# Performance work log

Hardware: AMD Instinct MI355X
Metric: run time of the kernel (lower is better)

The kernel has to match this reference:

```python
import jax, jax.numpy as jnp
import numpy as np

B, C, H, W = 4, 256, 64, 64
C8 = C // 8


def setup_inputs() -> dict:
    key = jax.random.key(0)
    ks = jax.random.split(key, 8)
    x = jax.random.normal(ks[0], (B, C, H, W), dtype=jnp.float32)
    # 1x1 conv weights act as per-pixel linear maps: [out_ch, in_ch]
    Wq = jax.random.normal(ks[1], (C8, C), dtype=jnp.float32) * 0.05
    bq = jax.random.normal(ks[2], (C8,), dtype=jnp.float32) * 0.01
    Wk = jax.random.normal(ks[3], (C8, C), dtype=jnp.float32) * 0.05
    bk = jax.random.normal(ks[4], (C8,), dtype=jnp.float32) * 0.01
    Wv = jax.random.normal(ks[5], (C, C), dtype=jnp.float32) * 0.05
    bv = jax.random.normal(ks[6], (C,), dtype=jnp.float32) * 0.01
    # torch inits gamma to 0 (identity); use nonzero so output exercises the attention path
    gamma = jnp.array(0.5, dtype=jnp.float32)
    return {"x": x, "Wq": Wq, "bq": bq, "Wk": Wk, "bk": bk, "Wv": Wv, "bv": bv, "gamma": gamma}


def reference(x, Wq, bq, Wk, bk, Wv, bv, gamma):
    b, c, h, w = x.shape
    n = h * w
    xf = x.reshape(b, c, n)                                   # [B,C,N]
    q = jnp.einsum('oc,bcn->bno', Wq, xf) + bq                # [B,N,C8] (proj_query permuted)
    k = jnp.einsum('oc,bcn->bon', Wk, xf) + bk[:, None]       # [B,C8,N]
    energy = jnp.einsum('bnc,bcm->bnm', q, k)                 # [B,N_q,N_k]
    # NOTE: torch Softmax(dim=1) -> normalize over the QUERY axis (axis=1)
    attention = jax.nn.softmax(energy, axis=1)
    v = jnp.einsum('oc,bcn->bon', Wv, xf) + bv[:, None]       # [B,C,N]
    out = jnp.einsum('bcn,bnm->bcm', v, attention).reshape(b, c, h, w)
    return gamma * out + x
```

## Files before the change

kernel.cpp:

```cpp
#include <hip/hip_runtime.h>
#include <hip/hip_bf16.h>

#define BN 4
#define CC 256
#define C8 32
#define NN 4096
#define PROJ_ROWS 320

typedef __attribute__((ext_vector_type(8))) short short8;
typedef __attribute__((ext_vector_type(4))) float f32x4;

__device__ __forceinline__ unsigned short f2bf(float f) {
    unsigned u = __builtin_bit_cast(unsigned, f);
    unsigned r = (u + 0x7fffu + ((u >> 16) & 1u)) >> 16;
    return (unsigned short)r;
}

__global__ __launch_bounds__(256) void proj_kernel(
    const float* __restrict__ x,
    const float* __restrict__ Wq, const float* __restrict__ bq,
    const float* __restrict__ Wk, const float* __restrict__ bk,
    const float* __restrict__ Wv, const float* __restrict__ bv,
    unsigned short* __restrict__ proj, unsigned short* __restrict__ qT)
{
    int bid = blockIdx.x;
    int b = bid >> 6, nt = bid & 63;
    int n0 = nt * 64;
    int tid = threadIdx.x;
    int w = tid >> 6, l = tid & 63, l15 = l & 15, lq = l >> 4;

    __shared__ alignas(16) unsigned short Xt[64][264];

    int c_l = tid >> 3;
    int nb  = (tid & 7) * 8;

#pragma unroll
    for (int kc = 0; kc < 8; kc++) {
        const float* xp = x + ((size_t)(b * CC + kc * 32 + c_l)) * NN + n0 + nb;
        float4 x0 = *(const float4*)xp;
        float4 x1 = *(const float4*)(xp + 4);
        float t[8] = {x0.x, x0.y, x0.z, x0.w, x1.x, x1.y, x1.z, x1.w};
#pragma unroll
        for (int e = 0; e < 8; e++) Xt[nb + e][kc * 32 + c_l] = f2bf(t[e]);
    }
    __syncthreads();

    f32x4 acc[5][4];
#pragma unroll
    for (int gi = 0; gi < 5; gi++)
#pragma unroll
        for (int mi = 0; mi < 4; mi++) acc[gi][mi] = (f32x4){0.f, 0.f, 0.f, 0.f};

    for (int kc = 0; kc < 8; kc++) {
        float4 wf[5][2];
#pragma unroll
        for (int gi = 0; gi < 5; gi++) {
            int og = (w * 5 + gi) * 16 + l15;
            const float* wrow = (og < 32) ? (Wq + (size_t)og * CC)
                              : (og < 64) ? (Wk + (size_t)(og - 32) * CC)
                                          : (Wv + (size_t)(og - 64) * CC);
            const float* wp = wrow + kc * 32 + lq * 8;
            wf[gi][0] = *(const float4*)wp;
            wf[gi][1] = *(const float4*)(wp + 4);
        }
#pragma unroll
        for (int gi = 0; gi < 5; gi++) {
            unsigned short a8[8] __attribute__((aligned(16)));
            float tw[8] = {wf[gi][0].x, wf[gi][0].y, wf[gi][0].z, wf[gi][0].w,
                           wf[gi][1].x, wf[gi][1].y, wf[gi][1].z, wf[gi][1].w};
#pragma unroll
            for (int e = 0; e < 8; e++) a8[e] = f2bf(tw[e]);
            short8 af = *(const short8*)a8;
#pragma unroll
            for (int mi = 0; mi < 4; mi++) {
                short8 bf = *(const short8*)&Xt[mi * 16 + l15][kc * 32 + lq * 8];
                acc[gi][mi] = __builtin_amdgcn_mfma_f32_16x16x32_bf16(af, bf, acc[gi][mi], 0, 0, 0);
            }
        }
    }

#pragma unroll
    for (int gi = 0; gi < 5; gi++) {
#pragma unroll
        for (int r = 0; r < 4; r++) {
            int og = (w * 5 + gi) * 16 + lq * 4 + r;
            float bias = (og < 32) ? bq[og] : (og < 64) ? bk[og - 32] : bv[og - 64];
#pragma unroll
            for (int mi = 0; mi < 4; mi++) {
                int n = n0 + mi * 16 + l15;
                unsigned short v16 = f2bf(acc[gi][mi][r] + bias);
                if (og < 32) {
                    qT[((size_t)b * NN + n) * C8 + og] = v16;
                } else {
                    proj[((size_t)b * PROJ_ROWS + og) * NN + n] = v16;
                }
            }
        }
    }
}

template<int NSPLIT, bool FINAL>
__global__ __launch_bounds__(256, 4) void attn_kernel(
    const unsigned short* __restrict__ proj,
    const unsigned short* __restrict__ qT,
    const float* __restrict__ x,
    const float* __restrict__ gamma_p,
    float* __restrict__ out,
    float* __restrict__ Opart,
    float* __restrict__ Lpart)
{
    constexpr int ITERS = 64 / NSPLIT;
    int bid = blockIdx.x;
    int h   = bid >> 8;
    int low = bid & 255;
    int xcd = low & 7;
    int b = xcd >> 1;
    int mtile = ((low >> 3) << 1) | (xcd & 1);
    int m0 = mtile * 64;
    int nbase = h * (ITERS * 64);

    int tid = threadIdx.x;
    int w = tid >> 6, l = tid & 63, l15 = l & 15, lq = l >> 4;

    __shared__ alignas(16) unsigned short ps[2][64][72];
    __shared__ float red[4][64];
    __shared__ float Ltot[64];

    const unsigned short* kbase = proj + ((size_t)b * PROJ_ROWS + C8) * NN;
    const unsigned short* vbase = proj + ((size_t)b * PROJ_ROWS + 64) * NN;
    const unsigned short* qbase = qT + (size_t)b * NN * C8;

    short8 kfrag[4];
#pragma unroll
    for (int mi = 0; mi < 4; mi++) {
        int col = m0 + mi * 16 + l15;
        unsigned short t8[8] __attribute__((aligned(16)));
#pragma unroll
        for (int j = 0; j < 8; j++)
            t8[j] = kbase[(size_t)(lq * 8 + j) * NN + col];
        kfrag[mi] = *(const short8*)t8;
    }

    f32x4 O[4][4];
#pragma unroll
    for (int ci = 0; ci < 4; ci++)
#pragma unroll
        for (int mi = 0; mi < 4; mi++) O[ci][mi] = (f32x4){0.f, 0.f, 0.f, 0.f};
    float runS[4] = {0.f, 0.f, 0.f, 0.f};

    {
        short8 qfrag = *(const short8*)(qbase + (size_t)(nbase + 16 * w + l15) * C8 + lq * 8);
#pragma unroll
        for (int mi = 0; mi < 4; mi++) {
            f32x4 S = __builtin_amdgcn_mfma_f32_16x16x32_bf16(
                qfrag, kfrag[mi], (f32x4){0.f, 0.f, 0.f, 0.f}, 0, 0, 0);
            float p0 = __expf(S[0]);
            float p1 = __expf(S[1]);
            float p2 = __expf(S[2]);
            float p3 = __expf(S[3]);
            runS[mi] += (p0 + p1) + (p2 + p3);
            unsigned pk0 = (unsigned)f2bf(p0) | ((unsigned)f2bf(p1) << 16);
            unsigned pk1 = (unsigned)f2bf(p2) | ((unsigned)f2bf(p3) << 16);
            *(uint2*)&ps[0][mi * 16 + l15][16 * w + lq * 4] = make_uint2(pk0, pk1);
        }
    }

    for (int it = 0; it < ITERS; it++) {
        int n0c = nbase + it * 64;
        __syncthreads();

        const unsigned short* psrc = &ps[it & 1][0][0];
#pragma unroll
        for (int kh = 0; kh < 2; kh++) {
            short8 av[4];
#pragma unroll
            for (int ci = 0; ci < 4; ci++)
                av[ci] = *(const short8*)(vbase
                         + (size_t)(64 * w + ci * 16 + l15) * NN + n0c + kh * 32 + lq * 8);
            short8 bfr[4];
#pragma unroll
            for (int mi = 0; mi < 4; mi++)
                bfr[mi] = *(const short8*)(psrc + (mi * 16 + l15) * 72 + kh * 32 + lq * 8);
#pragma unroll
            for (int ci = 0; ci < 4; ci++)
#pragma unroll
                for (int mi = 0; mi < 4; mi++)
                    O[ci][mi] = __builtin_amdgcn_mfma_f32_16x16x32_bf16(
                        av[ci], bfr[mi], O[ci][mi], 0, 0, 0);
        }

        if (it + 1 < ITERS) {
            short8 qfrag = *(const short8*)(qbase
                           + (size_t)(n0c + 64 + 16 * w + l15) * C8 + lq * 8);
            unsigned short* pdst = &ps[(it + 1) & 1][0][0];
#pragma unroll
            for (int mi = 0; mi < 4; mi++) {
                f32x4 S = __builtin_amdgcn_mfma_f32_16x16x32_bf16(
                    qfrag, kfrag[mi], (f32x4){0.f, 0.f, 0.f, 0.f}, 0, 0, 0);
                float p0 = __expf(S[0]);
                float p1 = __expf(S[1]);
                float p2 = __expf(S[2]);
                float p3 = __expf(S[3]);
                runS[mi] += (p0 + p1) + (p2 + p3);
                unsigned pk0 = (unsigned)f2bf(p0) | ((unsigned)f2bf(p1) << 16);
                unsigned pk1 = (unsigned)f2bf(p2) | ((unsigned)f2bf(p3) << 16);
                *(uint2*)(pdst + (mi * 16 + l15) * 72 + 16 * w + lq * 4) = make_uint2(pk0, pk1);
            }
        }
    }

#pragma unroll
    for (int mi = 0; mi < 4; mi++) {
        float s = runS[mi];
        s += __shfl_xor(s, 16);
        s += __shfl_xor(s, 32);
        red[w][mi * 16 + l15] = s;
    }
    __syncthreads();
    if (tid < 64) Ltot[tid] = red[0][tid] + red[1][tid] + red[2][tid] + red[3][tid];
    __syncthreads();

    if constexpr (FINAL) {
        float gamma = gamma_p[0];
        float iv[4];
#pragma unroll
        for (int mi = 0; mi < 4; mi++) iv[mi] = 1.0f / Ltot[mi * 16 + l15];
#pragma unroll
        for (int ci = 0; ci < 4; ci++) {
#pragma unroll
            for (int mi = 0; mi < 4; mi++) {
                int m = m0 + mi * 16 + l15;
#pragma unroll
                for (int r = 0; r < 4; r++) {
                    int c = 64 * w + ci * 16 + lq * 4 + r;
                    size_t idx = ((size_t)b * CC + c) * NN + m;
                    out[idx] = gamma * (O[ci][mi][r] * iv[mi]) + x[idx];
                }
            }
        }
    } else {
        size_t p = ((size_t)h * BN + b) * 64 + mtile;
        if (tid < 64) Lpart[p * 64 + tid] = Ltot[tid];
        float* Ob = Opart + p * (size_t)(CC * 64);
#pragma unroll
        for (int ci = 0; ci < 4; ci++) {
#pragma unroll
            for (int mi = 0; mi < 4; mi++) {
#pragma unroll
                for (int r = 0; r < 4; r++) {
                    int c = 64 * w + ci * 16 + lq * 4 + r;
                    Ob[c * 64 + mi * 16 + l15] = O[ci][mi][r];
                }
            }
        }
    }
}

template<int NSPLIT>
__global__ __launch_bounds__(256) void combine_kernel(
    const float* __restrict__ Opart, const float* __restrict__ Lpart,
    const float* __restrict__ x, const float* __restrict__ gamma_p,
    float* __restrict__ out)
{
    int bid = blockIdx.x;
    int cq = bid & 3;
    int mt = (bid >> 2) & 63;
    int b  = bid >> 8;
    int tid = threadIdx.x;
    int m4 = tid & 15, c16 = tid >> 4;
    float gamma = gamma_p[0];

    f32x4 Ls = (f32x4){0.f, 0.f, 0.f, 0.f};
#pragma unroll
    for (int h = 0; h < NSPLIT; h++) {
        size_t p = ((size_t)h * BN + b) * 64 + mt;
        Ls += *(const f32x4*)(Lpart + p * 64 + m4 * 4);
    }
    f32x4 inv;
#pragma unroll
    for (int j = 0; j < 4; j++) inv[j] = 1.0f / Ls[j];

#pragma unroll
    for (int cp = 0; cp < 4; cp++) {
        int c = cq * 64 + cp * 16 + c16;
        f32x4 acc = (f32x4){0.f, 0.f, 0.f, 0.f};
#pragma unroll
        for (int h = 0; h < NSPLIT; h++) {
            size_t p = ((size_t)h * BN + b) * 64 + mt;
            acc += *(const f32x4*)(Opart + p * (size_t)(CC * 64) + c * 64 + m4 * 4);
        }
        size_t idx = ((size_t)b * CC + c) * NN + mt * 64 + m4 * 4;
        f32x4 xv = *(const f32x4*)(x + idx);
        f32x4 o;
#pragma unroll
        for (int j = 0; j < 4; j++) o[j] = gamma * (acc[j] * inv[j]) + xv[j];
        *(f32x4*)(out + idx) = o;
    }
}

extern "C" void kernel_launch(void* const* d_in, const int* in_sizes, int n_in,
                              void* d_out, int out_size, void* d_ws, size_t ws_size,
                              hipStream_t stream) {
    const float* x     = (const float*)d_in[0];
    const float* Wq    = (const float*)d_in[1];
    const float* bq    = (const float*)d_in[2];
    const float* Wk    = (const float*)d_in[3];
    const float* bk    = (const float*)d_in[4];
    const float* Wv    = (const float*)d_in[5];
    const float* bv    = (const float*)d_in[6];
    const float* gamma = (const float*)d_in[7];
    float* out = (float*)d_out;
    (void)in_sizes; (void)n_in; (void)out_size;

    unsigned short* proj = (unsigned short*)d_ws;
    unsigned short* qT   = proj + (size_t)BN * PROJ_ROWS * NN;
    const size_t baseB = ((size_t)BN * PROJ_ROWS * NN + (size_t)BN * NN * C8) * 2;

    auto needB = [&](int ns) {
        size_t LpB = (size_t)ns * BN * 64 * 64 * 4;
        size_t OpB = (size_t)ns * BN * 64 * CC * 64 * 4;
        return baseB + LpB + OpB;
    };

    proj_kernel<<<256, 256, 0, stream>>>(x, Wq, bq, Wk, bk, Wv, bv, proj, qT);

    if (ws_size >= needB(4)) {
        float* Lpart = (float*)((char*)d_ws + baseB);
        float* Opart = Lpart + (size_t)4 * BN * 64 * 64;
        attn_kernel<4, false><<<1024, 256, 0, stream>>>(proj, qT, x, gamma, out, Opart, Lpart);
        combine_kernel<4><<<1024, 256, 0, stream>>>(Opart, Lpart, x, gamma, out);
    } else if (ws_size >= needB(2)) {
        float* Lpart = (float*)((char*)d_ws + baseB);
        float* Opart = Lpart + (size_t)2 * BN * 64 * 64;
        attn_kernel<2, false><<<512, 256, 0, stream>>>(proj, qT, x, gamma, out, Opart, Lpart);
        combine_kernel<2><<<1024, 256, 0, stream>>>(Opart, Lpart, x, gamma, out);
    } else {
        attn_kernel<1, true><<<256, 256, 0, stream>>>(proj, qT, x, gamma, out, nullptr, nullptr);
    }
}
```

Before: 181.7 us.

## Split attention 8-way, store partials in bf16, fold log2e into K, halve proj tiles

The attention split-K factor goes from 4 to 8 (2048 blocks), with launch bounds raised to 8 waves per SIMD, and partial outputs are stored as bf16 to cut combine traffic. K is pre-scaled by log2(e) in the projection so the softmax can use exp2f. The projection kernel uses 32-column tiles and 512 blocks for more parallelism. Risks: bf16 partial sums lose precision, the higher occupancy target may cause register spills, and the NSPLIT=2 fallback is removed.

```diff
diff --git a/kernel.cpp b/kernel.cpp
--- a/kernel.cpp
+++ b/kernel.cpp
@@ -6,6 +6,7 @@
 #define C8 32
 #define NN 4096
 #define PROJ_ROWS 320
+#define LOG2E 1.4426950408889634f
 
 typedef __attribute__((ext_vector_type(8))) short short8;
 typedef __attribute__((ext_vector_type(4))) float f32x4;
@@ -14,6 +15,12 @@
     unsigned u = __builtin_bit_cast(unsigned, f);
     unsigned r = (u + 0x7fffu + ((u >> 16) & 1u)) >> 16;
     return (unsigned short)r;
+}
+__device__ __forceinline__ float bfhi2f(unsigned u) {
+    return __builtin_bit_cast(float, u & 0xffff0000u);
+}
+__device__ __forceinline__ float bflo2f(unsigned u) {
+    return __builtin_bit_cast(float, u << 16);
 }
 
 __global__ __launch_bounds__(256) void proj_kernel(
@@ -24,32 +31,32 @@
     unsigned short* __restrict__ proj, unsigned short* __restrict__ qT)
 {
     int bid = blockIdx.x;
-    int b = bid >> 6, nt = bid & 63;
-    int n0 = nt * 64;
+    int b = bid >> 7, nt = bid & 127;
+    int n0 = nt * 32;
     int tid = threadIdx.x;
     int w = tid >> 6, l = tid & 63, l15 = l & 15, lq = l >> 4;
 
-    __shared__ alignas(16) unsigned short Xt[64][264];
+    __shared__ alignas(16) unsigned short Xt[32][264];
 
     int c_l = tid >> 3;
-    int nb  = (tid & 7) * 8;
+    int nb  = (tid & 7) * 4;
 
 #pragma unroll
     for (int kc = 0; kc < 8; kc++) {
         const float* xp = x + ((size_t)(b * CC + kc * 32 + c_l)) * NN + n0 + nb;
         float4 x0 = *(const float4*)xp;
-        float4 x1 = *(const float4*)(xp + 4);
-        float t[8] = {x0.x, x0.y, x0.z, x0.w, x1.x, x1.y, x1.z, x1.w};
-#pragma unroll
-        for (int e = 0; e < 8; e++) Xt[nb + e][kc * 32 + c_l] = f2bf(t[e]);
+        Xt[nb + 0][kc * 32 + c_l] = f2bf(x0.x);
+        Xt[nb + 1][kc * 32 + c_l] = f2bf(x0.y);
+        Xt[nb + 2][kc * 32 + c_l] = f2bf(x0.z);
+        Xt[nb + 3][kc * 32 + c_l] = f2bf(x0.w);
     }
     __syncthreads();
 
-    f32x4 acc[5][4];
+    f32x4 acc[5][2];
 #pragma unroll
     for (int gi = 0; gi < 5; gi++)
 #pragma unroll
-        for (int mi = 0; mi < 4; mi++) acc[gi][mi] = (f32x4){0.f, 0.f, 0.f, 0.f};
+        for (int mi = 0; mi < 2; mi++) acc[gi][mi] = (f32x4){0.f, 0.f, 0.f, 0.f};
 
     for (int kc = 0; kc < 8; kc++) {
         float4 wf[5][2];
@@ -72,7 +79,7 @@
             for (int e = 0; e < 8; e++) a8[e] = f2bf(tw[e]);
             short8 af = *(const short8*)a8;
 #pragma unroll
-            for (int mi = 0; mi < 4; mi++) {
+            for (int mi = 0; mi < 2; mi++) {
                 short8 bf = *(const short8*)&Xt[mi * 16 + l15][kc * 32 + lq * 8];
                 acc[gi][mi] = __builtin_amdgcn_mfma_f32_16x16x32_bf16(af, bf, acc[gi][mi], 0, 0, 0);
             }
@@ -85,10 +92,13 @@
         for (int r = 0; r < 4; r++) {
             int og = (w * 5 + gi) * 16 + lq * 4 + r;
             float bias = (og < 32) ? bq[og] : (og < 64) ? bk[og - 32] : bv[og - 64];
-#pragma unroll
-            for (int mi = 0; mi < 4; mi++) {
+            bool is_k = (og >= 32) && (og < 64);
+#pragma unroll
+            for (int mi = 0; mi < 2; mi++) {
                 int n = n0 + mi * 16 + l15;
-                unsigned short v16 = f2bf(acc[gi][mi][r] + bias);
+                float v = acc[gi][mi][r] + bias;
+                if (is_k) v *= LOG2E;
+                unsigned short v16 = f2bf(v);
                 if (og < 32) {
                     qT[((size_t)b * NN + n) * C8 + og] = v16;
                 } else {
@@ -100,13 +110,13 @@
 }
 
 template<int NSPLIT, bool FINAL>
-__global__ __launch_bounds__(256, 4) void attn_kernel(
+__global__ __launch_bounds__(256, 8) void attn_kernel(
     const unsigned short* __restrict__ proj,
     const unsigned short* __restrict__ qT,
     const float* __restrict__ x,
     const float* __restrict__ gamma_p,
     float* __restrict__ out,
-    float* __restrict__ Opart,
+    unsigned short* __restrict__ Opart,
     float* __restrict__ Lpart)
 {
     constexpr int ITERS = 64 / NSPLIT;
@@ -154,10 +164,10 @@
         for (int mi = 0; mi < 4; mi++) {
             f32x4 S = __builtin_amdgcn_mfma_f32_16x16x32_bf16(
                 qfrag, kfrag[mi], (f32x4){0.f, 0.f, 0.f, 0.f}, 0, 0, 0);
-            float p0 = __expf(S[0]);
-            float p1 = __expf(S[1]);
-            float p2 = __expf(S[2]);
-            float p3 = __expf(S[3]);
+            float p0 = exp2f(S[0]);
+            float p1 = exp2f(S[1]);
+            float p2 = exp2f(S[2]);
+            float p3 = exp2f(S[3]);
             runS[mi] += (p0 + p1) + (p2 + p3);
             unsigned pk0 = (unsigned)f2bf(p0) | ((unsigned)f2bf(p1) << 16);
             unsigned pk1 = (unsigned)f2bf(p2) | ((unsigned)f2bf(p3) << 16);
@@ -197,10 +207,10 @@
             for (int mi = 0; mi < 4; mi++) {
                 f32x4 S = __builtin_amdgcn_mfma_f32_16x16x32_bf16(
                     qfrag, kfrag[mi], (f32x4){0.f, 0.f, 0.f, 0.f}, 0, 0, 0);
-                float p0 = __expf(S[0]);
-                float p1 = __expf(S[1]);
-                float p2 = __expf(S[2]);
-                float p3 = __expf(S[3]);
+                float p0 = exp2f(S[0]);
+                float p1 = exp2f(S[1]);
+                float p2 = exp2f(S[2]);
+                float p3 = exp2f(S[3]);
                 runS[mi] += (p0 + p1) + (p2 + p3);
                 unsigned pk0 = (unsigned)f2bf(p0) | ((unsigned)f2bf(p1) << 16);
                 unsigned pk1 = (unsigned)f2bf(p2) | ((unsigned)f2bf(p3) << 16);
@@ -241,7 +251,7 @@
     } else {
         size_t p = ((size_t)h * BN + b) * 64 + mtile;
         if (tid < 64) Lpart[p * 64 + tid] = Ltot[tid];
-        float* Ob = Opart + p * (size_t)(CC * 64);
+        unsigned short* Ob = Opart + p * (size_t)(CC * 64);
 #pragma unroll
         for (int ci = 0; ci < 4; ci++) {
 #pragma unroll
@@ -249,7 +259,7 @@
 #pragma unroll
                 for (int r = 0; r < 4; r++) {
                     int c = 64 * w + ci * 16 + lq * 4 + r;
-                    Ob[c * 64 + mi * 16 + l15] = O[ci][mi][r];
+                    Ob[c * 64 + mi * 16 + l15] = f2bf(O[ci][mi][r]);
                 }
             }
         }
@@ -258,7 +268,7 @@
 
 template<int NSPLIT>
 __global__ __launch_bounds__(256) void combine_kernel(
-    const float* __restrict__ Opart, const float* __restrict__ Lpart,
+    const unsigned short* __restrict__ Opart, const float* __restrict__ Lpart,
     const float* __restrict__ x, const float* __restrict__ gamma_p,
     float* __restrict__ out)
 {
@@ -287,7 +297,11 @@
 #pragma unroll
         for (int h = 0; h < NSPLIT; h++) {
             size_t p = ((size_t)h * BN + b) * 64 + mt;
-            acc += *(const f32x4*)(Opart + p * (size_t)(CC * 64) + c * 64 + m4 * 4);
+            uint2 u = *(const uint2*)(Opart + p * (size_t)(CC * 64) + c * 64 + m4 * 4);
+            acc[0] += bflo2f(u.x);
+            acc[1] += bfhi2f(u.x);
+            acc[2] += bflo2f(u.y);
+            acc[3] += bfhi2f(u.y);
         }
         size_t idx = ((size_t)b * CC + c) * NN + mt * 64 + m4 * 4;
         f32x4 xv = *(const f32x4*)(x + idx);
@@ -316,24 +330,24 @@
     unsigned short* qT   = proj + (size_t)BN * PROJ_ROWS * NN;
     const size_t baseB = ((size_t)BN * PROJ_ROWS * NN + (size_t)BN * NN * C8) * 2;
 
-    auto needB = [&](int ns) {
-        size_t LpB = (size_t)ns * BN * 64 * 64 * 4;
-        size_t OpB = (size_t)ns * BN * 64 * CC * 64 * 4;
+    auto needB = [&](size_t ns) {
+        size_t LpB = ns * BN * 64 * 64 * 4;
+        size_t OpB = ns * BN * 64 * (size_t)(CC * 64) * 2;
         return baseB + LpB + OpB;
     };
 
-    proj_kernel<<<256, 256, 0, stream>>>(x, Wq, bq, Wk, bk, Wv, bv, proj, qT);
-
-    if (ws_size >= needB(4)) {
+    proj_kernel<<<512, 256, 0, stream>>>(x, Wq, bq, Wk, bk, Wv, bv, proj, qT);
+
+    if (ws_size >= needB(8)) {
         float* Lpart = (float*)((char*)d_ws + baseB);
-        float* Opart = Lpart + (size_t)4 * BN * 64 * 64;
+        unsigned short* Opart = (unsigned short*)(Lpart + (size_t)8 * BN * 64 * 64);
+        attn_kernel<8, false><<<2048, 256, 0, stream>>>(proj, qT, x, gamma, out, Opart, Lpart);
+        combine_kernel<8><<<1024, 256, 0, stream>>>(Opart, Lpart, x, gamma, out);
+    } else if (ws_size >= needB(4)) {
+        float* Lpart = (float*)((char*)d_ws + baseB);
+        unsigned short* Opart = (unsigned short*)(Lpart + (size_t)4 * BN * 64 * 64);
         attn_kernel<4, false><<<1024, 256, 0, stream>>>(proj, qT, x, gamma, out, Opart, Lpart);
         combine_kernel<4><<<1024, 256, 0, stream>>>(Opart, Lpart, x, gamma, out);
-    } else if (ws_size >= needB(2)) {
-        float* Lpart = (float*)((char*)d_ws + baseB);
-        float* Opart = Lpart + (size_t)2 * BN * 64 * 64;
-        attn_kernel<2, false><<<512, 256, 0, stream>>>(proj, qT, x, gamma, out, Opart, Lpart);
-        combine_kernel<2><<<1024, 256, 0, stream>>>(Opart, Lpart, x, gamma, out);
     } else {
         attn_kernel<1, true><<<256, 256, 0, stream>>>(proj, qT, x, gamma, out, nullptr, nullptr);
     }
```

Measured after the change: 620.6 us. +241.6%, slower.
